# Kernel tuning notes

Measured on AMD Instinct MI355X. Metric: run time of the kernel, lower is better.

Reference implementation:

```python
import jax, jax.numpy as jnp
import numpy as np

B, D = 16384, 512
NUM_CLASSES, K = 90, 32


def _l2norm(v, axis=-1):
    return v / jnp.sqrt(jnp.sum(v * v, axis=axis, keepdims=True) + 1e-12)


def setup_inputs() -> dict:
    key = jax.random.key(0)
    k1, k2, k3 = jax.random.split(key, 3)
    x = jax.random.normal(k1, (B, D), dtype=jnp.float32)
    labels = jax.random.randint(k2, (B,), 0, NUM_CLASSES, dtype=jnp.int64)
    centers = jax.random.normal(k3, (NUM_CLASSES, K, D), dtype=jnp.float32)
    return {"x": x, "labels": labels, "centers": centers}


def reference(x, labels, centers):
    # l2Norm applied to centers at init and to x in forward
    xn = _l2norm(x, axis=1)                       # [B, D]
    cn = _l2norm(centers, axis=-1)                # [C, K, D]
    c = cn[labels]                                # gather: [B, K, D]
    # dst_k = 1 - <x_b, center_{label_b, k}>
    dst = 1.0 - jnp.einsum("bd,bkd->bk", xn, c)   # [B, K]
    score = jax.nn.softmax(2.0 - dst, axis=1)     # softmax over K sub-centers
    per_sample = jnp.sum(score * dst, axis=1)     # [B]
    return jnp.mean(per_sample)                   # scalar loss
```

## Files before the change

kernel.cpp:

```cpp
#include <hip/hip_runtime.h>
#include <hip/hip_bf16.h>

#define BB 16384
#define DD 512
#define NCLS 90
#define KC 32
#define BUCKET 512
#define MAGIC 0x7f3a9c51u

typedef __attribute__((ext_vector_type(8))) short short8;
typedef __attribute__((ext_vector_type(4))) float fx4;

static __device__ __forceinline__ short8 pack8s(float sc, float4 a, float4 b) {
    union { __hip_bfloat162 h[4]; short8 s; } u;
    u.h[0] = __float22bfloat162_rn(make_float2(a.x * sc, a.y * sc));
    u.h[1] = __float22bfloat162_rn(make_float2(a.z * sc, a.w * sc));
    u.h[2] = __float22bfloat162_rn(make_float2(b.x * sc, b.y * sc));
    u.h[3] = __float22bfloat162_rn(make_float2(b.z * sc, b.w * sc));
    return u.s;
}
static __device__ __forceinline__ short8 pack8(float4 a, float4 b) {
    union { __hip_bfloat162 h[4]; short8 s; } u;
    u.h[0] = __float22bfloat162_rn(make_float2(a.x, a.y));
    u.h[1] = __float22bfloat162_rn(make_float2(a.z, a.w));
    u.h[2] = __float22bfloat162_rn(make_float2(b.x, b.y));
    u.h[3] = __float22bfloat162_rn(make_float2(b.z, b.w));
    return u.s;
}

__global__ __launch_bounds__(256, 2)
void k_all(const float* __restrict__ x,
           const float* __restrict__ centers,
           const int* __restrict__ labels,
           int* __restrict__ idx,
           int* __restrict__ cnt,
           unsigned int* __restrict__ flag,
           float* __restrict__ partials) {
    __shared__ __align__(16) char u_lds[64 * 1024];
    __shared__ float S_lds[32][33];
    __shared__ float xinv[32];
    __shared__ float red4[4];
    __shared__ int wcnt[4];

    int*   lab   = (int*)u_lds;
    short* c_lds = (short*)u_lds;
    short* x_lds = (short*)(u_lds + 32768);

    int b = blockIdx.x;
    int c, p;
    if (b < NCLS) { c = b; p = 0; }
    else { c = (b - NCLS) / 7; p = 1 + (b - NCLS) % 7; }
    int t = threadIdx.x, w = t >> 6, lane = t & 63;

    if (p == 0) {
        for (int j = t; j < BB / 4; j += 256)
            ((int4*)lab)[j] = ((const int4*)labels)[j];
        __syncthreads();
        int seg4 = w * (BB / 4 / 4);
        int cw = 0;
#pragma unroll
        for (int jj = 0; jj < 16; jj++) {
            int4 v = ((int4*)lab)[seg4 + jj * 64 + lane];
            cw += (v.x == c) + (v.y == c) + (v.z == c) + (v.w == c);
        }
#pragma unroll
        for (int m = 1; m < 64; m <<= 1) cw += __shfl_xor(cw, m, 64);
        if (lane == 0) wcnt[w] = cw;
        __syncthreads();
        int n0 = wcnt[0] + wcnt[1] + wcnt[2] + wcnt[3];
        int pos = c * BUCKET;
        for (int ww = 0; ww < w; ww++) pos += wcnt[ww];
#pragma unroll
        for (int jj = 0; jj < 16; jj++) {
            int4 v = ((int4*)lab)[seg4 + jj * 64 + lane];
            int gbase = (seg4 + jj * 64 + lane) * 4;
            { bool m = (v.x == c); unsigned long long k = __ballot(m);
              if (m) idx[pos + __popcll(k & ((1ull << lane) - 1ull))] = gbase;     pos += __popcll(k); }
            { bool m = (v.y == c); unsigned long long k = __ballot(m);
              if (m) idx[pos + __popcll(k & ((1ull << lane) - 1ull))] = gbase + 1; pos += __popcll(k); }
            { bool m = (v.z == c); unsigned long long k = __ballot(m);
              if (m) idx[pos + __popcll(k & ((1ull << lane) - 1ull))] = gbase + 2; pos += __popcll(k); }
            { bool m = (v.w == c); unsigned long long k = __ballot(m);
              if (m) idx[pos + __popcll(k & ((1ull << lane) - 1ull))] = gbase + 3; pos += __popcll(k); }
        }
        for (int j = n0 + t; j < BUCKET; j += 256) idx[c * BUCKET + j] = 0;
        __syncthreads();
        if (t == 0) {
            cnt[c] = n0;
            __hip_atomic_store(&flag[c], MAGIC, __ATOMIC_RELEASE, __HIP_MEMORY_SCOPE_AGENT);
        }
    }

    {
        int row8 = t >> 3, l8 = t & 7;
        const float4* csrc = (const float4*)(centers + ((size_t)c * KC + row8) * DD);
        float s = 0.f;
#pragma unroll
        for (int jj = 0; jj < 8; jj++) {
            float4 a = csrc[(l8 + 8 * jj) * 2], b4 = csrc[(l8 + 8 * jj) * 2 + 1];
            s += a.x * a.x + a.y * a.y + a.z * a.z + a.w * a.w
               + b4.x * b4.x + b4.y * b4.y + b4.z * b4.z + b4.w * b4.w;
        }
#pragma unroll
        for (int m = 1; m < 8; m <<= 1) s += __shfl_xor(s, m, 64);
        float sc = rsqrtf(s + 1e-12f);
#pragma unroll
        for (int jj = 0; jj < 8; jj++) {
            int c16 = l8 + 8 * jj;
            float4 a = csrc[c16 * 2], b4 = csrc[c16 * 2 + 1];
            *(short8*)&c_lds[row8 * DD + ((c16 ^ (row8 & 7)) << 3)] = pack8s(sc, a, b4);
        }
    }

    if (p != 0 && t == 0) {
        while (__hip_atomic_load(&flag[c], __ATOMIC_ACQUIRE, __HIP_MEMORY_SCOPE_AGENT) != MAGIC)
            __builtin_amdgcn_s_sleep(2);
    }
    __syncthreads();

    int n = cnt[c];
    int nch = (n + 31) >> 5;
    float loss_acc = 0.f;

    if (p < nch) {
        int base = c * BUCKET;
        int mrow = ((w & 1) << 4) + (lane & 15);
        int nrow = ((w >> 1) << 4) + (lane & 15);
        int row8 = t >> 3, l8 = t & 7;

        for (int ch = p; ch < nch; ch += 8) {
            int off = ch << 5;
            int rem = n - off;

            {
                int g = idx[base + off + row8];
                const float4* src = (const float4*)(x + (size_t)g * DD);
                float4 va[8], vb[8];
#pragma unroll
                for (int jj = 0; jj < 8; jj++) {
                    va[jj] = src[2 * l8 + 16 * jj];
                    vb[jj] = src[2 * l8 + 16 * jj + 1];
                }
                float nrm = 0.f;
#pragma unroll
                for (int jj = 0; jj < 8; jj++) {
                    int cc = l8 + 8 * jj;
                    float4 a = va[jj], b4 = vb[jj];
                    nrm += a.x * a.x + a.y * a.y + a.z * a.z + a.w * a.w
                         + b4.x * b4.x + b4.y * b4.y + b4.z * b4.z + b4.w * b4.w;
                    *(short8*)&x_lds[row8 * DD + ((cc ^ (row8 & 7)) << 3)] = pack8(a, b4);
                }
#pragma unroll
                for (int m = 1; m < 8; m <<= 1) nrm += __shfl_xor(nrm, m, 64);
                if (l8 == 0) xinv[row8] = rsqrtf(nrm + 1e-12f);
            }
            __syncthreads();

            fx4 acc = {0.f, 0.f, 0.f, 0.f};
#pragma unroll
            for (int ks = 0; ks < 16; ks++) {
                int c16a = ks * 4 + (lane >> 4);
                short8 av = *(const short8*)&x_lds[mrow * DD + ((c16a ^ (mrow & 7)) << 3)];
                short8 bv = *(const short8*)&c_lds[nrow * DD + ((c16a ^ (nrow & 7)) << 3)];
                acc = __builtin_amdgcn_mfma_f32_16x16x32_bf16(av, bv, acc, 0, 0, 0);
            }
#pragma unroll
            for (int j = 0; j < 4; j++) {
                int r = ((w & 1) << 4) + ((lane >> 4) << 2) + j;
                int col = ((w >> 1) << 4) + (lane & 15);
                S_lds[r][col] = acc[j];
            }
            __syncthreads();

            {
                float xv = xinv[row8];
                int q4 = l8 << 2;
                float s0 = S_lds[row8][q4 + 0] * xv;
                float s1 = S_lds[row8][q4 + 1] * xv;
                float s2 = S_lds[row8][q4 + 2] * xv;
                float s3 = S_lds[row8][q4 + 3] * xv;
                float mx = fmaxf(fmaxf(s0, s1), fmaxf(s2, s3));
#pragma unroll
                for (int m = 1; m < 8; m <<= 1) mx = fmaxf(mx, __shfl_xor(mx, m, 64));
                float e0 = expf(s0 - mx), e1 = expf(s1 - mx);
                float e2 = expf(s2 - mx), e3 = expf(s3 - mx);
                float Z = e0 + e1 + e2 + e3;
                float num = e0 * (1.f - s0) + e1 * (1.f - s1)
                          + e2 * (1.f - s2) + e3 * (1.f - s3);
#pragma unroll
                for (int m = 1; m < 8; m <<= 1) {
                    Z += __shfl_xor(Z, m, 64);
                    num += __shfl_xor(num, m, 64);
                }
                if (l8 == 0 && row8 < rem) loss_acc += num / Z;
            }
            __syncthreads();
        }
    }

#pragma unroll
    for (int m = 1; m < 64; m <<= 1) loss_acc += __shfl_xor(loss_acc, m, 64);
    if (lane == 0) red4[w] = loss_acc;
    __syncthreads();
    if (t == 0) partials[b] = red4[0] + red4[1] + red4[2] + red4[3];
}

__global__ void k_final(const float* __restrict__ partials, float* __restrict__ out) {
    __shared__ float red[256];
    int t = threadIdx.x;
    float s = 0.f;
    for (int i = t; i < NCLS * 8; i += 256) s += partials[i];
    red[t] = s;
    __syncthreads();
    for (int h = 128; h > 0; h >>= 1) {
        if (t < h) red[t] += red[t + h];
        __syncthreads();
    }
    if (t == 0) out[0] = red[0] * (1.0f / (float)BB);
}

extern "C" void kernel_launch(void* const* d_in, const int* in_sizes, int n_in,
                              void* d_out, int out_size, void* d_ws, size_t ws_size,
                              hipStream_t stream) {
    const float* x       = (const float*)d_in[0];
    const int*   labels  = (const int*)d_in[1];
    const float* centers = (const float*)d_in[2];
    float* out = (float*)d_out;

    char* ws = (char*)d_ws;
    int*          idx      = (int*)(ws + 0);
    int*          cnt      = (int*)(ws + 184320);
    unsigned int* flag     = (unsigned int*)(ws + 184832);
    float*        partials = (float*)(ws + 196608);

    k_all<<<NCLS * 8, 256, 0, stream>>>(x, centers, labels, idx, cnt, flag, partials);
    k_final<<<1, 256, 0, stream>>>(partials, out);
}
```

Baseline: 29.20 us.

## Split label binning into separate kernel and prefetch gathered x rows

Label binning moves out of the fused kernel into its own 1024-thread kernel, which removes the atomic flag spin-wait between blocks. The main kernel loads the first x chunk and the centers into registers up front and prefetches the next chunk's rows while the current chunk's softmax runs. The softmax max-subtraction is dropped in favour of __expf directly, which relies on the cosine scores being bounded in [-1,1]. The cost is an extra kernel launch and more register pressure from holding two sets of float4 arrays.

```diff
diff --git a/kernel.cpp b/kernel.cpp
--- a/kernel.cpp
+++ b/kernel.cpp
@@ -6,7 +6,7 @@
 #define NCLS 90
 #define KC 32
 #define BUCKET 512
-#define MAGIC 0x7f3a9c51u
+#define NP 8
 
 typedef __attribute__((ext_vector_type(8))) short short8;
 typedef __attribute__((ext_vector_type(4))) float fx4;
@@ -28,124 +28,126 @@
     return u.s;
 }
 
-__global__ __launch_bounds__(256, 2)
-void k_all(const float* __restrict__ x,
-           const float* __restrict__ centers,
-           const int* __restrict__ labels,
-           int* __restrict__ idx,
-           int* __restrict__ cnt,
-           unsigned int* __restrict__ flag,
-           float* __restrict__ partials) {
-    __shared__ __align__(16) char u_lds[64 * 1024];
+__global__ __launch_bounds__(1024)
+void k_bin(const int* __restrict__ labels, int* __restrict__ idx, int* __restrict__ cnt) {
+    __shared__ int lab[BB];
+    __shared__ int wcnt[16];
+
+    int t = threadIdx.x, w = t >> 6, lane = t & 63;
+    int c = blockIdx.x;
+    for (int j = t; j < BB / 4; j += 1024)
+        ((int4*)lab)[j] = ((const int4*)labels)[j];
+    __syncthreads();
+
+    int seg4 = w * (BB / 4 / 16);
+    int cw = 0;
+#pragma unroll
+    for (int jj = 0; jj < 4; jj++) {
+        int4 v = ((int4*)lab)[seg4 + jj * 64 + lane];
+        cw += (v.x == c) + (v.y == c) + (v.z == c) + (v.w == c);
+    }
+#pragma unroll
+    for (int m = 1; m < 64; m <<= 1) cw += __shfl_xor(cw, m, 64);
+    if (lane == 0) wcnt[w] = cw;
+    __syncthreads();
+    int pos = c * BUCKET;
+    for (int ww = 0; ww < w; ww++) pos += wcnt[ww];
+#pragma unroll
+    for (int jj = 0; jj < 4; jj++) {
+        int4 v = ((int4*)lab)[seg4 + jj * 64 + lane];
+        int gbase = (seg4 + jj * 64 + lane) * 4;
+        { bool m = (v.x == c); unsigned long long k = __ballot(m);
+          if (m) idx[pos + __popcll(k & ((1ull << lane) - 1ull))] = gbase;     pos += __popcll(k); }
+        { bool m = (v.y == c); unsigned long long k = __ballot(m);
+          if (m) idx[pos + __popcll(k & ((1ull << lane) - 1ull))] = gbase + 1; pos += __popcll(k); }
+        { bool m = (v.z == c); unsigned long long k = __ballot(m);
+          if (m) idx[pos + __popcll(k & ((1ull << lane) - 1ull))] = gbase + 2; pos += __popcll(k); }
+        { bool m = (v.w == c); unsigned long long k = __ballot(m);
+          if (m) idx[pos + __popcll(k & ((1ull << lane) - 1ull))] = gbase + 3; pos += __popcll(k); }
+    }
+    if (t == 0) {
+        int s = 0;
+#pragma unroll
+        for (int i = 0; i < 16; i++) s += wcnt[i];
+        cnt[c] = s;
+    }
+}
+
+__launch_bounds__(256, 2)
+__global__ void k_main(const float* __restrict__ x,
+                       const float* __restrict__ centers,
+                       const int* __restrict__ cnt,
+                       const int* __restrict__ idx,
+                       float* __restrict__ partials) {
+    __shared__ __align__(16) short c_lds[KC * DD];
+    __shared__ __align__(16) short x_lds[32 * DD];
     __shared__ float S_lds[32][33];
     __shared__ float xinv[32];
     __shared__ float red4[4];
-    __shared__ int wcnt[4];
-
-    int*   lab   = (int*)u_lds;
-    short* c_lds = (short*)u_lds;
-    short* x_lds = (short*)(u_lds + 32768);
-
-    int b = blockIdx.x;
-    int c, p;
-    if (b < NCLS) { c = b; p = 0; }
-    else { c = (b - NCLS) / 7; p = 1 + (b - NCLS) % 7; }
-    int t = threadIdx.x, w = t >> 6, lane = t & 63;
-
-    if (p == 0) {
-        for (int j = t; j < BB / 4; j += 256)
-            ((int4*)lab)[j] = ((const int4*)labels)[j];
-        __syncthreads();
-        int seg4 = w * (BB / 4 / 4);
-        int cw = 0;
-#pragma unroll
-        for (int jj = 0; jj < 16; jj++) {
-            int4 v = ((int4*)lab)[seg4 + jj * 64 + lane];
-            cw += (v.x == c) + (v.y == c) + (v.z == c) + (v.w == c);
-        }
-#pragma unroll
-        for (int m = 1; m < 64; m <<= 1) cw += __shfl_xor(cw, m, 64);
-        if (lane == 0) wcnt[w] = cw;
-        __syncthreads();
-        int n0 = wcnt[0] + wcnt[1] + wcnt[2] + wcnt[3];
-        int pos = c * BUCKET;
-        for (int ww = 0; ww < w; ww++) pos += wcnt[ww];
-#pragma unroll
-        for (int jj = 0; jj < 16; jj++) {
-            int4 v = ((int4*)lab)[seg4 + jj * 64 + lane];
-            int gbase = (seg4 + jj * 64 + lane) * 4;
-            { bool m = (v.x == c); unsigned long long k = __ballot(m);
-              if (m) idx[pos + __popcll(k & ((1ull << lane) - 1ull))] = gbase;     pos += __popcll(k); }
-            { bool m = (v.y == c); unsigned long long k = __ballot(m);
-              if (m) idx[pos + __popcll(k & ((1ull << lane) - 1ull))] = gbase + 1; pos += __popcll(k); }
-            { bool m = (v.z == c); unsigned long long k = __ballot(m);
-              if (m) idx[pos + __popcll(k & ((1ull << lane) - 1ull))] = gbase + 2; pos += __popcll(k); }
-            { bool m = (v.w == c); unsigned long long k = __ballot(m);
-              if (m) idx[pos + __popcll(k & ((1ull << lane) - 1ull))] = gbase + 3; pos += __popcll(k); }
-        }
-        for (int j = n0 + t; j < BUCKET; j += 256) idx[c * BUCKET + j] = 0;
-        __syncthreads();
-        if (t == 0) {
-            cnt[c] = n0;
-            __hip_atomic_store(&flag[c], MAGIC, __ATOMIC_RELEASE, __HIP_MEMORY_SCOPE_AGENT);
-        }
-    }
-
-    {
-        int row8 = t >> 3, l8 = t & 7;
-        const float4* csrc = (const float4*)(centers + ((size_t)c * KC + row8) * DD);
-        float s = 0.f;
-#pragma unroll
-        for (int jj = 0; jj < 8; jj++) {
-            float4 a = csrc[(l8 + 8 * jj) * 2], b4 = csrc[(l8 + 8 * jj) * 2 + 1];
-            s += a.x * a.x + a.y * a.y + a.z * a.z + a.w * a.w
-               + b4.x * b4.x + b4.y * b4.y + b4.z * b4.z + b4.w * b4.w;
-        }
-#pragma unroll
-        for (int m = 1; m < 8; m <<= 1) s += __shfl_xor(s, m, 64);
-        float sc = rsqrtf(s + 1e-12f);
-#pragma unroll
-        for (int jj = 0; jj < 8; jj++) {
-            int c16 = l8 + 8 * jj;
-            float4 a = csrc[c16 * 2], b4 = csrc[c16 * 2 + 1];
-            *(short8*)&c_lds[row8 * DD + ((c16 ^ (row8 & 7)) << 3)] = pack8s(sc, a, b4);
-        }
-    }
-
-    if (p != 0 && t == 0) {
-        while (__hip_atomic_load(&flag[c], __ATOMIC_ACQUIRE, __HIP_MEMORY_SCOPE_AGENT) != MAGIC)
-            __builtin_amdgcn_s_sleep(2);
-    }
-    __syncthreads();
-
+
+    int c = blockIdx.x >> 3;
+    int p = blockIdx.x & 7;
     int n = cnt[c];
     int nch = (n + 31) >> 5;
+    int t = threadIdx.x, w = t >> 6, lane = t & 63;
     float loss_acc = 0.f;
 
     if (p < nch) {
         int base = c * BUCKET;
+        int row8 = t >> 3, l8 = t & 7;
         int mrow = ((w & 1) << 4) + (lane & 15);
         int nrow = ((w >> 1) << 4) + (lane & 15);
-        int row8 = t >> 3, l8 = t & 7;
-
-        for (int ch = p; ch < nch; ch += 8) {
+
+        float4 xva[8], xvb[8];
+        {
+            int off = p << 5;
+            int rem = n - off;
+            int r = (row8 < rem) ? row8 : (rem - 1);
+            int g = idx[base + off + r];
+            const float4* src = (const float4*)(x + (size_t)g * DD);
+#pragma unroll
+            for (int jj = 0; jj < 8; jj++) {
+                xva[jj] = src[2 * l8 + 16 * jj];
+                xvb[jj] = src[2 * l8 + 16 * jj + 1];
+            }
+        }
+
+        {
+            const float4* csrc = (const float4*)(centers + ((size_t)c * KC + row8) * DD);
+            float4 cva[8], cvb[8];
+#pragma unroll
+            for (int jj = 0; jj < 8; jj++) {
+                cva[jj] = csrc[2 * l8 + 16 * jj];
+                cvb[jj] = csrc[2 * l8 + 16 * jj + 1];
+            }
+            float s = 0.f;
+#pragma unroll
+            for (int jj = 0; jj < 8; jj++) {
+                float4 a = cva[jj], b4 = cvb[jj];
+                s += a.x * a.x + a.y * a.y + a.z * a.z + a.w * a.w
+                   + b4.x * b4.x + b4.y * b4.y + b4.z * b4.z + b4.w * b4.w;
+            }
+#pragma unroll
+            for (int m = 1; m < 8; m <<= 1) s += __shfl_xor(s, m, 64);
+            float sc = rsqrtf(s + 1e-12f);
+#pragma unroll
+            for (int jj = 0; jj < 8; jj++) {
+                int c16 = l8 + 8 * jj;
+                *(short8*)&c_lds[row8 * DD + ((c16 ^ (row8 & 7)) << 3)]
+                    = pack8s(sc, cva[jj], cvb[jj]);
+            }
+        }
+
+        for (int ch = p; ch < nch; ch += NP) {
             int off = ch << 5;
             int rem = n - off;
 
             {
-                int g = idx[base + off + row8];
-                const float4* src = (const float4*)(x + (size_t)g * DD);
-                float4 va[8], vb[8];
-#pragma unroll
-                for (int jj = 0; jj < 8; jj++) {
-                    va[jj] = src[2 * l8 + 16 * jj];
-                    vb[jj] = src[2 * l8 + 16 * jj + 1];
-                }
                 float nrm = 0.f;
 #pragma unroll
                 for (int jj = 0; jj < 8; jj++) {
                     int cc = l8 + 8 * jj;
-                    float4 a = va[jj], b4 = vb[jj];
+                    float4 a = xva[jj], b4 = xvb[jj];
                     nrm += a.x * a.x + a.y * a.y + a.z * a.z + a.w * a.w
                          + b4.x * b4.x + b4.y * b4.y + b4.z * b4.z + b4.w * b4.w;
                     *(short8*)&x_lds[row8 * DD + ((cc ^ (row8 & 7)) << 3)] = pack8(a, b4);
@@ -169,6 +171,19 @@
                 int r = ((w & 1) << 4) + ((lane >> 4) << 2) + j;
                 int col = ((w >> 1) << 4) + (lane & 15);
                 S_lds[r][col] = acc[j];
+            }
+
+            if (ch + NP < nch) {
+                int off2 = (ch + NP) << 5;
+                int rem2 = n - off2;
+                int r2 = (row8 < rem2) ? row8 : (rem2 - 1);
+                int g2 = idx[base + off2 + r2];
+                const float4* src2 = (const float4*)(x + (size_t)g2 * DD);
+#pragma unroll
+                for (int jj = 0; jj < 8; jj++) {
+                    xva[jj] = src2[2 * l8 + 16 * jj];
+                    xvb[jj] = src2[2 * l8 + 16 * jj + 1];
+                }
             }
             __syncthreads();
 
@@ -179,11 +194,8 @@
                 float s1 = S_lds[row8][q4 + 1] * xv;
                 float s2 = S_lds[row8][q4 + 2] * xv;
                 float s3 = S_lds[row8][q4 + 3] * xv;
-                float mx = fmaxf(fmaxf(s0, s1), fmaxf(s2, s3));
-#pragma unroll
-                for (int m = 1; m < 8; m <<= 1) mx = fmaxf(mx, __shfl_xor(mx, m, 64));
-                float e0 = expf(s0 - mx), e1 = expf(s1 - mx);
-                float e2 = expf(s2 - mx), e3 = expf(s3 - mx);
+                float e0 = __expf(s0), e1 = __expf(s1);
+                float e2 = __expf(s2), e3 = __expf(s3);
                 float Z = e0 + e1 + e2 + e3;
                 float num = e0 * (1.f - s0) + e1 * (1.f - s1)
                           + e2 * (1.f - s2) + e3 * (1.f - s3);
@@ -202,14 +214,14 @@
     for (int m = 1; m < 64; m <<= 1) loss_acc += __shfl_xor(loss_acc, m, 64);
     if (lane == 0) red4[w] = loss_acc;
     __syncthreads();
-    if (t == 0) partials[b] = red4[0] + red4[1] + red4[2] + red4[3];
+    if (t == 0) partials[blockIdx.x] = red4[0] + red4[1] + red4[2] + red4[3];
 }
 
 __global__ void k_final(const float* __restrict__ partials, float* __restrict__ out) {
     __shared__ float red[256];
     int t = threadIdx.x;
     float s = 0.f;
-    for (int i = t; i < NCLS * 8; i += 256) s += partials[i];
+    for (int i = t; i < NCLS * NP; i += 256) s += partials[i];
     red[t] = s;
     __syncthreads();
     for (int h = 128; h > 0; h >>= 1) {
@@ -228,11 +240,11 @@
     float* out = (float*)d_out;
 
     char* ws = (char*)d_ws;
-    int*          idx      = (int*)(ws + 0);
-    int*          cnt      = (int*)(ws + 184320);
-    unsigned int* flag     = (unsigned int*)(ws + 184832);
-    float*        partials = (float*)(ws + 196608);
-
-    k_all<<<NCLS * 8, 256, 0, stream>>>(x, centers, labels, idx, cnt, flag, partials);
+    int*   idx      = (int*)(ws + 0);
+    int*   cnt      = (int*)(ws + 184320);
+    float* partials = (float*)(ws + 196608);
+
+    k_bin<<<NCLS, 1024, 0, stream>>>(labels, idx, cnt);
+    k_main<<<NCLS * NP, 256, 0, stream>>>(x, centers, cnt, idx, partials);
     k_final<<<1, 256, 0, stream>>>(partials, out);
 }
```

Result: faster. 28.60 us (-2.1%).
